# Optimization experiments

Measured on AMD Instinct MI355X. Metric: run time of the kernel, lower is better.

## Reference

```python
import jax, jax.numpy as jnp
import numpy as np

N = 100000      # nodes
E = 3200000     # edges
D_IN = 16
D_OUT = 32
DIM = 3         # pseudo-coordinate dimensionality
K = 2           # kernel_size per dim
NUM_K = K ** DIM  # 8 spline kernel weight matrices
BN_EPS = 1e-5


def _spline_basis(pseudo):
    """Degree-1 open B-spline basis, kernel_size=2 per dim.

    v = pseudo * (K - degree) = pseudo, so for pseudo in [0,1) floor(v)=0 and
    frac = pseudo; per-dim basis over the 2 knots is (1-frac, frac). The full
    basis over all 2^DIM kernel weights is the outer product across dims,
    flattened with flat index = i0 + 2*i1 + 4*i2.
    Returns [E, 2^DIM].
    """
    frac = pseudo  # [E, DIM]
    e = pseudo.shape[0]
    basis = jnp.ones((e, 1), pseudo.dtype)
    for d in range(DIM):
        b_d = jnp.stack([1.0 - frac[:, d], frac[:, d]], axis=1)  # [E, 2]
        # new flat index = i_d * prev_size + prev_index
        basis = (basis[:, None, :] * b_d[:, :, None]).reshape(e, -1)
    return basis  # [E, NUM_K]


def setup_inputs() -> dict:
    key = jax.random.key(0)
    ks = jax.random.split(key, 6)
    x = jax.random.normal(ks[0], (N, D_IN), dtype=jnp.float32)
    edge_index = jax.random.randint(ks[1], (2, E), 0, N, dtype=jnp.int32)
    edge_attr = jax.random.uniform(ks[2], (E, DIM), dtype=jnp.float32)
    # learned params
    W = jax.random.normal(ks[3], (NUM_K, D_IN, D_OUT), dtype=jnp.float32) * 0.1
    W_root = jax.random.normal(ks[4], (D_IN, D_OUT), dtype=jnp.float32) * 0.1
    bias = jnp.zeros((D_OUT,), jnp.float32)
    gamma = jnp.ones((D_OUT,), jnp.float32)
    beta = jnp.zeros((D_OUT,), jnp.float32)
    return dict(x=x, edge_index=edge_index, edge_attr=edge_attr,
                W=W, W_root=W_root, bias=bias, gamma=gamma, beta=beta)


def reference(x, edge_index, edge_attr, W, W_root, bias, gamma, beta):
    src, dst = edge_index[0], edge_index[1]
    basis = _spline_basis(edge_attr)          # [E, 8]
    x_j = x[src]                              # [E, d_in] per-edge gather
    # basis-weighted linear combination over the 8 kernel weights
    msg = jnp.zeros((x_j.shape[0], D_OUT), x.dtype)
    for k in range(NUM_K):                    # fixed small loop over kernels
        msg = msg + basis[:, k:k + 1] * (x_j @ W[k])
    # scatter-mean to target nodes (SplineConv default aggr='mean')
    agg = jax.ops.segment_sum(msg, dst, num_segments=N)
    cnt = jax.ops.segment_sum(jnp.ones((msg.shape[0],), x.dtype), dst, num_segments=N)
    agg = agg / jnp.maximum(cnt, 1.0)[:, None]
    out = agg + x @ W_root + bias             # root weight + bias
    out = jax.nn.elu(out)                     # activation
    # BatchNorm over the node dimension (training mode: batch statistics)
    mean = out.mean(axis=0)
    var = out.var(axis=0)
    out = (out - mean) * jax.lax.rsqrt(var + BN_EPS) * gamma + beta
    return out
```

## Files before the change

kernel.cpp:

```cpp
#include <hip/hip_runtime.h>
#include <math.h>

#define TPB 256
#define FTPB 512
#define D_IN 16
#define D_OUT 32
#define NUM_K 8
#define WPAD 516
#define SBN_LOG 9
#define SBN 512
#define CT 4096
#define EPT 16

__global__ void k_init(int* __restrict__ sbase, int* __restrict__ scursor,
                       int* __restrict__ sbcnt, int cap, int strided) {
    int t = threadIdx.x;
    if (t < 257) sbase[t] = strided ? t * cap : 0;
    if (t < 256) { scursor[t] = 0; sbcnt[t] = 0; }
}


__global__ void k_sbhist(const int* __restrict__ dst, int* __restrict__ sbcnt, int E) {
    __shared__ int h[256];
    for (int i = threadIdx.x; i < 256; i += TPB) h[i] = 0;
    __syncthreads();
    int stride = gridDim.x * TPB;
    for (int e = blockIdx.x * TPB + threadIdx.x; e < E; e += stride)
        atomicAdd(&h[dst[e] >> SBN_LOG], 1);
    __syncthreads();
    for (int i = threadIdx.x; i < 256; i += TPB)
        if (h[i]) atomicAdd(&sbcnt[i], h[i]);
}

__global__ void k_sbscan(const int* __restrict__ sbcnt, int* __restrict__ sbase, int nsb) {
    __shared__ int sd[256];
    int t = threadIdx.x;
    int own = (t < nsb) ? sbcnt[t] : 0;
    sd[t] = own;
    __syncthreads();
    for (int s = 1; s < 256; s <<= 1) {
        int add = (t >= s) ? sd[t - s] : 0;
        __syncthreads();
        sd[t] += add;
        __syncthreads();
    }
    sbase[t] = sd[t] - own;
}

__global__ __launch_bounds__(TPB) void k_coarse(
        const int* __restrict__ src, const int* __restrict__ dst,
        const float* __restrict__ attr, const int* __restrict__ sbase,
        int* __restrict__ scursor, uint2* __restrict__ tmp, int E, int nsb) {
    __shared__ int hist[256];
    __shared__ int base[256];
    __shared__ int goff[256];
    __shared__ __align__(16) uint2 stage[CT];
    __shared__ unsigned char ssb[CT];

    int tile0 = blockIdx.x * CT;
    for (int i = threadIdx.x; i < 256; i += TPB) hist[i] = 0;
    __syncthreads();

    unsigned rx[EPT], ry[EPT];
    int rk[EPT], sbv[EPT];
#pragma unroll
    for (int i = 0; i < EPT; i++) {
        int e = tile0 + i * TPB + threadIdx.x;
        sbv[i] = -1;
        if (e < E) {
            int s = src[e], d = dst[e];
            float f0 = attr[3 * e + 0], f1 = attr[3 * e + 1], f2 = attr[3 * e + 2];
            int q0 = min((int)(f0 * 1024.f), 1023);
            int q1 = min((int)(f1 * 1024.f), 1023);
            int q2 = min((int)(f2 * 1024.f), 1023);
            int sb = d >> SBN_LOG;
            rx[i] = (unsigned)s | ((unsigned)(d & (SBN - 1)) << 17);
            ry[i] = (unsigned)q0 | ((unsigned)q1 << 10) | ((unsigned)q2 << 20);
            rk[i] = atomicAdd(&hist[sb], 1);
            sbv[i] = sb;
        }
    }
    __syncthreads();

    int t = threadIdx.x;
    int cntv = hist[t];
    base[t] = cntv;
    __syncthreads();
    for (int s = 1; s < 256; s <<= 1) {
        int add = (t >= s) ? base[t - s] : 0;
        __syncthreads();
        base[t] += add;
        __syncthreads();
    }
    int excl = base[t] - cntv;
    if (t < nsb && cntv > 0) goff[t] = sbase[t] + atomicAdd(&scursor[t], cntv);
    __syncthreads();
    base[t] = excl;
    __syncthreads();

#pragma unroll
    for (int i = 0; i < EPT; i++) {
        if (sbv[i] >= 0) {
            int slot = base[sbv[i]] + rk[i];
            stage[slot] = make_uint2(rx[i], ry[i]);
            ssb[slot] = (unsigned char)sbv[i];
        }
    }
    __syncthreads();

    int tileCount = min(E - tile0, CT);
    for (int j = threadIdx.x; j < tileCount; j += TPB) {
        int sb = ssb[j];
        tmp[goff[sb] + (j - base[sb])] = stage[j];
    }
}

__global__ __launch_bounds__(FTPB) void k_fine2(
        const uint2* __restrict__ tmp, const int* __restrict__ sbase,
        const int* __restrict__ scursor, int* __restrict__ rs, int* __restrict__ re,
        uint2* __restrict__ rec, int N) {
    __shared__ int hist[SBN];
    __shared__ int wsum[8], woff[8];
    int b = blockIdx.x;
    int lo = sbase[b];
    int hi = lo + scursor[b];
    int t = threadIdx.x;
    hist[t] = 0;
    __syncthreads();
    for (int p = lo + t; p < hi; p += FTPB)
        atomicAdd(&hist[(tmp[p].x >> 17) & (SBN - 1)], 1);
    __syncthreads();
    int own = hist[t];

    int lane = t & 63, w = t >> 6;
    int inc = own;
#pragma unroll
    for (int s = 1; s < 64; s <<= 1) {
        int u = __shfl_up(inc, s);
        if (lane >= s) inc += u;
    }
    if (lane == 63) wsum[w] = inc;
    __syncthreads();
    if (t < 8) {
        int x = wsum[t], ex = x;
#pragma unroll
        for (int s = 1; s < 8; s <<= 1) {
            int u = __shfl_up(ex, s);
            if (t >= s) ex += u;
        }
        woff[t] = ex - x;
    }
    __syncthreads();
    int incl = inc + woff[w];
    int excl = incl - own;

    int n = (b << SBN_LOG) + t;
    if (n < N) { rs[n] = lo + excl; re[n] = lo + incl; }
    hist[t] = lo + excl;
    __syncthreads();
    for (int p = lo + t; p < hi; p += FTPB) {
        uint2 r = tmp[p];
        int dl = (int)((r.x >> 17) & (SBN - 1));
        int slot = atomicAdd(&hist[dl], 1);
        rec[slot] = make_uint2(r.x & 0x1FFFFu, r.y);
    }
}


__global__ void k_zero(int* __restrict__ cnt, int N) {
    int i = blockIdx.x * TPB + threadIdx.x;
    if (i < N) cnt[i] = 0;
}

__global__ void k_hist(const int* __restrict__ dst, int* __restrict__ cnt, int E) {
    int e = blockIdx.x * TPB + threadIdx.x;
    if (e < E) atomicAdd(&cnt[dst[e]], 1);
}

__global__ void k_scan_a(const int* __restrict__ cnt, int* __restrict__ bsum, int N) {
    __shared__ int sd[TPB];
    int i = blockIdx.x * TPB + threadIdx.x;
    sd[threadIdx.x] = (i < N) ? cnt[i] : 0;
    __syncthreads();
    for (int s = TPB / 2; s > 0; s >>= 1) {
        if (threadIdx.x < s) sd[threadIdx.x] += sd[threadIdx.x + s];
        __syncthreads();
    }
    if (threadIdx.x == 0) bsum[blockIdx.x] = sd[0];
}

__global__ void k_scan_b(const int* __restrict__ bsum, int* __restrict__ boff, int nb) {
    __shared__ int sd[512];
    int t = threadIdx.x;
    int own = (t < nb) ? bsum[t] : 0;
    sd[t] = own;
    __syncthreads();
    for (int s = 1; s < 512; s <<= 1) {
        int a = sd[t];
        int b = (t >= s) ? sd[t - s] : 0;
        __syncthreads();
        sd[t] = a + b;
        __syncthreads();
    }
    if (t < nb) boff[t] = sd[t] - own;
}

__global__ void k_scan_c(const int* __restrict__ cnt, const int* __restrict__ boff,
                         int* __restrict__ rs, int* __restrict__ re, int N) {
    __shared__ int sd[TPB];
    int t = threadIdx.x;
    int i = blockIdx.x * TPB + t;
    int v = (i < N) ? cnt[i] : 0;
    sd[t] = v;
    __syncthreads();
    for (int s = 1; s < TPB; s <<= 1) {
        int a = sd[t];
        int b = (t >= s) ? sd[t - s] : 0;
        __syncthreads();
        sd[t] = a + b;
        __syncthreads();
    }
    int excl = sd[t] - v + boff[blockIdx.x];
    if (i < N) { rs[i] = excl; re[i] = excl; }
}

__global__ void k_scatter(const int* __restrict__ src, const int* __restrict__ dst,
                          const float* __restrict__ attr, int* __restrict__ re,
                          uint2* __restrict__ rec, int E) {
    int e = blockIdx.x * TPB + threadIdx.x;
    if (e < E) {
        float f0 = attr[3 * e + 0], f1 = attr[3 * e + 1], f2 = attr[3 * e + 2];
        int q0 = min((int)(f0 * 1024.f), 1023);
        int q1 = min((int)(f1 * 1024.f), 1023);
        int q2 = min((int)(f2 * 1024.f), 1023);
        unsigned pk = (unsigned)q0 | ((unsigned)q1 << 10) | ((unsigned)q2 << 20);
        int pos = atomicAdd(&re[dst[e]], 1);
        rec[pos] = make_uint2((unsigned)src[e], pk);
    }
}


__global__ __launch_bounds__(TPB, 4) void k_agg(
    const float* __restrict__ x, const float* __restrict__ W,
    const float* __restrict__ Wr, const float* __restrict__ bias,
    const int* __restrict__ rs, const int* __restrict__ re,
    const uint2* __restrict__ rec,
    float* __restrict__ out, float* __restrict__ partials, int N) {

    __shared__ __align__(16) float sW[NUM_K * WPAD];
    __shared__ __align__(16) float sWr[D_IN * D_OUT];
    __shared__ float sB[D_OUT];
    __shared__ float4 sStats[4][16];

    for (int idx = threadIdx.x; idx < NUM_K * D_IN * D_OUT; idx += TPB) {
        int k = idx >> 9, rem = idx & 511, i = rem >> 5, c = rem & 31;
        sW[k * WPAD + i * 32 + c] = W[idx];
    }
    for (int idx = threadIdx.x; idx < D_IN * D_OUT; idx += TPB) sWr[idx] = Wr[idx];
    if (threadIdx.x < D_OUT) sB[threadIdx.x] = bias[threadIdx.x];
    __syncthreads();

    int t   = blockIdx.x * TPB + threadIdx.x;
    int n   = t >> 4;
    int sub = t & 15;
    int grp = sub >> 3;
    int h   = sub & 7;
    bool valid = n < N;

    const float INV = 1.0f / 1024.0f, HLF = 1.0f / 2048.0f;
    float sc0 = (h & 1) ? INV : -INV, cc0 = (h & 1) ? HLF : 1.f - HLF;
    float sc1 = (h & 2) ? INV : -INV, cc1 = (h & 2) ? HLF : 1.f - HLF;
    float sc2 = (h & 4) ? INV : -INV, cc2 = (h & 4) ? HLF : 1.f - HLF;

    float4 g0 = {0,0,0,0}, g1 = {0,0,0,0}, g2 = {0,0,0,0}, g3 = {0,0,0,0};
    int deg = 0;
    if (valid) {
        int p0 = rs[n], p1 = re[n];
        deg = p1 - p0;
        int p = p0 + grp;
        if (p < p1) {
            int last = p1 - 1;
            uint2 r  = rec[p];
            uint2 rn = rec[min(p + 2, last)];
            const float4* xr = (const float4*)x + (size_t)r.x * 4;
            float4 xq0 = xr[0], xq1 = xr[1], xq2 = xr[2], xq3 = xr[3];
            for (; p < p1; p += 2) {
                uint2 rnn = rec[min(p + 4, last)];
                const float4* xnr = (const float4*)x + (size_t)rn.x * 4;
                float4 xn0 = xnr[0], xn1 = xnr[1], xn2 = xnr[2], xn3 = xnr[3];
                float q0v = (float)(r.y & 1023u);
                float q1v = (float)((r.y >> 10) & 1023u);
                float q2v = (float)((r.y >> 20) & 1023u);
                float bs = fmaf(q0v, sc0, cc0) * fmaf(q1v, sc1, cc1) * fmaf(q2v, sc2, cc2);
                g0.x = fmaf(bs, xq0.x, g0.x); g0.y = fmaf(bs, xq0.y, g0.y);
                g0.z = fmaf(bs, xq0.z, g0.z); g0.w = fmaf(bs, xq0.w, g0.w);
                g1.x = fmaf(bs, xq1.x, g1.x); g1.y = fmaf(bs, xq1.y, g1.y);
                g1.z = fmaf(bs, xq1.z, g1.z); g1.w = fmaf(bs, xq1.w, g1.w);
                g2.x = fmaf(bs, xq2.x, g2.x); g2.y = fmaf(bs, xq2.y, g2.y);
                g2.z = fmaf(bs, xq2.z, g2.z); g2.w = fmaf(bs, xq2.w, g2.w);
                g3.x = fmaf(bs, xq3.x, g3.x); g3.y = fmaf(bs, xq3.y, g3.y);
                g3.z = fmaf(bs, xq3.z, g3.z); g3.w = fmaf(bs, xq3.w, g3.w);
                r = rn; rn = rnn;
                xq0 = xn0; xq1 = xn1; xq2 = xn2; xq3 = xn3;
            }
        }
    }

    g0.x += __shfl_xor(g0.x, 8); g0.y += __shfl_xor(g0.y, 8);
    g0.z += __shfl_xor(g0.z, 8); g0.w += __shfl_xor(g0.w, 8);
    g1.x += __shfl_xor(g1.x, 8); g1.y += __shfl_xor(g1.y, 8);
    g1.z += __shfl_xor(g1.z, 8); g1.w += __shfl_xor(g1.w, 8);
    g2.x += __shfl_xor(g2.x, 8); g2.y += __shfl_xor(g2.y, 8);
    g2.z += __shfl_xor(g2.z, 8); g2.w += __shfl_xor(g2.w, 8);
    g3.x += __shfl_xor(g3.x, 8); g3.y += __shfl_xor(g3.y, 8);
    g3.z += __shfl_xor(g3.z, 8); g3.w += __shfl_xor(g3.w, 8);

    float4 o0 = {0,0,0,0}, o1 = {0,0,0,0}, o2 = {0,0,0,0}, o3 = {0,0,0,0};
    const float* wbase = sW + h * WPAD + grp * 16;
#define CONTRACT1(gv, i) { \
        const float4* wr_ = (const float4*)(wbase + (i) * 32); \
        float4 w0 = wr_[0], w1 = wr_[1], w2 = wr_[2], w3 = wr_[3]; \
        o0.x = fmaf(gv, w0.x, o0.x); o0.y = fmaf(gv, w0.y, o0.y); \
        o0.z = fmaf(gv, w0.z, o0.z); o0.w = fmaf(gv, w0.w, o0.w); \
        o1.x = fmaf(gv, w1.x, o1.x); o1.y = fmaf(gv, w1.y, o1.y); \
        o1.z = fmaf(gv, w1.z, o1.z); o1.w = fmaf(gv, w1.w, o1.w); \
        o2.x = fmaf(gv, w2.x, o2.x); o2.y = fmaf(gv, w2.y, o2.y); \
        o2.z = fmaf(gv, w2.z, o2.z); o2.w = fmaf(gv, w2.w, o2.w); \
        o3.x = fmaf(gv, w3.x, o3.x); o3.y = fmaf(gv, w3.y, o3.y); \
        o3.z = fmaf(gv, w3.z, o3.z); o3.w = fmaf(gv, w3.w, o3.w); }
    CONTRACT1(g0.x,  0) CONTRACT1(g0.y,  1) CONTRACT1(g0.z,  2) CONTRACT1(g0.w,  3)
    CONTRACT1(g1.x,  4) CONTRACT1(g1.y,  5) CONTRACT1(g1.z,  6) CONTRACT1(g1.w,  7)
    CONTRACT1(g2.x,  8) CONTRACT1(g2.y,  9) CONTRACT1(g2.z, 10) CONTRACT1(g2.w, 11)
    CONTRACT1(g3.x, 12) CONTRACT1(g3.y, 13) CONTRACT1(g3.z, 14) CONTRACT1(g3.w, 15)
#undef CONTRACT1

    float inv = 1.f / (float)(deg > 0 ? deg : 1);
    o0.x *= inv; o0.y *= inv; o0.z *= inv; o0.w *= inv;
    o1.x *= inv; o1.y *= inv; o1.z *= inv; o1.w *= inv;
    o2.x *= inv; o2.y *= inv; o2.z *= inv; o2.w *= inv;
    o3.x *= inv; o3.y *= inv; o3.z *= inv; o3.w *= inv;

    bool hi4 = (h & 4) != 0;
    float4 k0, k1, s0, s1;
    k0 = hi4 ? o2 : o0; k1 = hi4 ? o3 : o1;
    s0 = hi4 ? o0 : o2; s1 = hi4 ? o1 : o3;
    k0.x += __shfl_xor(s0.x, 4); k0.y += __shfl_xor(s0.y, 4);
    k0.z += __shfl_xor(s0.z, 4); k0.w += __shfl_xor(s0.w, 4);
    k1.x += __shfl_xor(s1.x, 4); k1.y += __shfl_xor(s1.y, 4);
    k1.z += __shfl_xor(s1.z, 4); k1.w += __shfl_xor(s1.w, 4);

    bool hi2 = (h & 2) != 0;
    float4 m0 = hi2 ? k1 : k0;
    float4 sm = hi2 ? k0 : k1;
    m0.x += __shfl_xor(sm.x, 2); m0.y += __shfl_xor(sm.y, 2);
    m0.z += __shfl_xor(sm.z, 2); m0.w += __shfl_xor(sm.w, 2);

    bool hi1 = (h & 1) != 0;
    float e0 = hi1 ? m0.z : m0.x;
    float e1 = hi1 ? m0.w : m0.y;
    float sa = hi1 ? m0.x : m0.z;
    float sb_ = hi1 ? m0.y : m0.w;
    e0 += __shfl_xor(sa, 1);
    e1 += __shfl_xor(sb_, 1);

    int c0 = 2 * sub;
    if (valid) {
        const float4* xr = (const float4*)x + (size_t)n * 4;
        float4 r0 = xr[0], r1 = xr[1], r2 = xr[2], r3 = xr[3];
#define ROOT1(xv, i) { \
            float2 w = *(const float2*)(sWr + (i) * 32 + c0); \
            e0 = fmaf(xv, w.x, e0); e1 = fmaf(xv, w.y, e1); }
        ROOT1(r0.x,  0) ROOT1(r0.y,  1) ROOT1(r0.z,  2) ROOT1(r0.w,  3)
        ROOT1(r1.x,  4) ROOT1(r1.y,  5) ROOT1(r1.z,  6) ROOT1(r1.w,  7)
        ROOT1(r2.x,  8) ROOT1(r2.y,  9) ROOT1(r2.z, 10) ROOT1(r2.w, 11)
        ROOT1(r3.x, 12) ROOT1(r3.y, 13) ROOT1(r3.z, 14) ROOT1(r3.w, 15)
#undef ROOT1
    }

    float2 bb = *(const float2*)(sB + c0);
    e0 += bb.x; e1 += bb.y;
    e0 = e0 > 0.f ? e0 : (__expf(e0) - 1.f);
    e1 = e1 > 0.f ? e1 : (__expf(e1) - 1.f);

    if (valid) *(float2*)(out + (size_t)n * D_OUT + c0) = make_float2(e0, e1);

    float ss0 = valid ? e0 : 0.f, ss1 = valid ? e1 : 0.f;
    float q0 = ss0 * ss0, q1 = ss1 * ss1;
    ss0 += __shfl_xor(ss0, 16); ss1 += __shfl_xor(ss1, 16);
    q0  += __shfl_xor(q0, 16);  q1  += __shfl_xor(q1, 16);
    ss0 += __shfl_xor(ss0, 32); ss1 += __shfl_xor(ss1, 32);
    q0  += __shfl_xor(q0, 32);  q1  += __shfl_xor(q1, 32);
    if ((threadIdx.x & 63) < 16)
        sStats[threadIdx.x >> 6][sub] = make_float4(ss0, ss1, q0, q1);
    __syncthreads();
    if (threadIdx.x < 64) {
        const float* sf = (const float*)sStats;
        float v = sf[threadIdx.x] + sf[64 + threadIdx.x] +
                  sf[128 + threadIdx.x] + sf[192 + threadIdx.x];
        int ssub = threadIdx.x >> 2, comp = threadIdx.x & 3;
        int col = 2 * ssub + (comp & 1) + 32 * (comp >> 1);
        partials[(size_t)blockIdx.x * 64 + col] = v;
    }
}


__global__ void k_red1(const float* __restrict__ partials, float* __restrict__ partials2,
                       int nrows) {
    __shared__ float sd[4][64];
    int col = threadIdx.x & 63, j = threadIdx.x >> 6;
    float v = 0.f;
    for (int k = 0; k < 16; k++) {
        int r = blockIdx.x * 64 + j * 16 + k;
        if (r < nrows) v += partials[(size_t)r * 64 + col];
    }
    sd[j][col] = v;
    __syncthreads();
    if (threadIdx.x < 64)
        partials2[(size_t)blockIdx.x * 64 + threadIdx.x] =
            sd[0][threadIdx.x] + sd[1][threadIdx.x] + sd[2][threadIdx.x] + sd[3][threadIdx.x];
}

__global__ void k_bnfin(const float* __restrict__ partials2, const float* __restrict__ gamma,
                        const float* __restrict__ beta, float* __restrict__ stats,
                        int nrows2, int N) {
    __shared__ float sd[2][64];
    int col = threadIdx.x & 63, j = threadIdx.x >> 6;
    float v = 0.f;
    for (int r = j; r < nrows2; r += 2) v += partials2[(size_t)r * 64 + col];
    sd[j][col] = v;
    __syncthreads();
    if (threadIdx.x < 32) {
        int c = threadIdx.x;
        float S = sd[0][c] + sd[1][c];
        float Q = sd[0][32 + c] + sd[1][32 + c];
        float mean = S / (float)N;
        float var  = Q / (float)N - mean * mean;
        float sc   = gamma[c] * rsqrtf(var + 1e-5f);
        stats[c]      = sc;
        stats[32 + c] = beta[c] - mean * sc;
    }
}

__global__ void k_bnapply(float* __restrict__ out, const float* __restrict__ stats, int total4) {
    int i = blockIdx.x * TPB + threadIdx.x;
    if (i < total4) {
        float4 v = ((float4*)out)[i];
        int c0 = (i * 4) & (D_OUT - 1);
        v.x = v.x * stats[c0 + 0] + stats[32 + c0 + 0];
        v.y = v.y * stats[c0 + 1] + stats[32 + c0 + 1];
        v.z = v.z * stats[c0 + 2] + stats[32 + c0 + 2];
        v.w = v.w * stats[c0 + 3] + stats[32 + c0 + 3];
        ((float4*)out)[i] = v;
    }
}


extern "C" void kernel_launch(void* const* d_in, const int* in_sizes, int n_in,
                              void* d_out, int out_size, void* d_ws, size_t ws_size,
                              hipStream_t stream) {
    const float* x     = (const float*)d_in[0];
    const int* eidx    = (const int*)d_in[1];
    const float* attr  = (const float*)d_in[2];
    const float* W     = (const float*)d_in[3];
    const float* Wr    = (const float*)d_in[4];
    const float* bias  = (const float*)d_in[5];
    const float* gamma = (const float*)d_in[6];
    const float* beta  = (const float*)d_in[7];
    float* out = (float*)d_out;

    const int N = in_sizes[0] / D_IN;
    const int E = in_sizes[1] / 2;
    const int* src = eidx;
    const int* dst = eidx + E;

    const int nb  = (N + TPB - 1) / TPB;
    const int gE  = (E + TPB - 1) / TPB;
    const int nsb = (N + SBN - 1) / SBN;
    const int nbAgg = (16 * N + TPB - 1) / TPB;
    const int nbRed = (nbAgg + 63) / 64;
    const int gC  = (E + CT - 1) / CT;

    int capBase = (E + nsb - 1) / nsb;
    int slack = capBase / 16 > 1024 ? capBase / 16 : 1024;
    int cap = capBase + slack;

    int* rs          = (int*)d_ws;
    int* re          = rs + N;
    float* partials  = (float*)(re + N);
    float* partials2 = partials + (size_t)nbAgg * 64;
    float* stats     = partials2 + (size_t)nbRed * 64;
    int* sbase       = (int*)(stats + 64);
    int* scursor     = sbase + 257;
    int* sbcnt       = scursor + 256;
    uintptr_t tail   = ((uintptr_t)(sbcnt + 256) + 15) & ~(uintptr_t)15;
    size_t headBytes = tail - (uintptr_t)d_ws;

    size_t recStr      = (size_t)nsb * cap;
    size_t needStrided = headBytes + 2 * recStr * 8;
    size_t needDense   = headBytes + 2 * (size_t)E * 8;
    size_t needSingle  = headBytes + (size_t)E * 8 + ((size_t)N + 2 * (size_t)nb) * 4;

    if (ws_size >= needStrided && nsb <= 256) {
        uint2* rec = (uint2*)tail;
        uint2* tmp = rec + recStr;
        k_init<<<1, 512, 0, stream>>>(sbase, scursor, sbcnt, cap, 1);
        k_coarse<<<gC, TPB, 0, stream>>>(src, dst, attr, sbase, scursor, tmp, E, nsb);
        k_fine2<<<nsb, FTPB, 0, stream>>>(tmp, sbase, scursor, rs, re, rec, N);
        k_agg<<<nbAgg, TPB, 0, stream>>>(x, W, Wr, bias, rs, re, rec, out, partials, N);
    } else if (ws_size >= needDense && nsb <= 256) {
        uint2* rec = (uint2*)tail;
        uint2* tmp = rec + E;
        k_init<<<1, 512, 0, stream>>>(sbase, scursor, sbcnt, cap, 0);
        int gH = min(1024, gE);
        k_sbhist<<<gH, TPB, 0, stream>>>(dst, sbcnt, E);
        k_sbscan<<<1, 256, 0, stream>>>(sbcnt, sbase, nsb);
        k_coarse<<<gC, TPB, 0, stream>>>(src, dst, attr, sbase, scursor, tmp, E, nsb);
        k_fine2<<<nsb, FTPB, 0, stream>>>(tmp, sbase, scursor, rs, re, rec, N);
        k_agg<<<nbAgg, TPB, 0, stream>>>(x, W, Wr, bias, rs, re, rec, out, partials, N);
    } else if (ws_size >= needSingle && nb <= 512) {
        uint2* rec = (uint2*)tail;
        int* cnt   = (int*)(rec + E);
        int* bsum  = cnt + N;
        int* boff  = bsum + nb;
        k_zero<<<nb, TPB, 0, stream>>>(cnt, N);
        k_hist<<<gE, TPB, 0, stream>>>(dst, cnt, E);
        k_scan_a<<<nb, TPB, 0, stream>>>(cnt, bsum, N);
        k_scan_b<<<1, 512, 0, stream>>>(bsum, boff, nb);
        k_scan_c<<<nb, TPB, 0, stream>>>(cnt, boff, rs, re, N);
        k_scatter<<<gE, TPB, 0, stream>>>(src, dst, attr, re, rec, E);
        k_agg<<<nbAgg, TPB, 0, stream>>>(x, W, Wr, bias, rs, re, rec, out, partials, N);
    }

    k_red1<<<nbRed, TPB, 0, stream>>>(partials, partials2, nbAgg);
    k_bnfin<<<1, 128, 0, stream>>>(partials2, gamma, beta, stats, nbRed, N);
    int total4 = N * D_OUT / 4;
    k_bnapply<<<(total4 + TPB - 1) / TPB, TPB, 0, stream>>>(out, stats, total4);
}
```

Before: 193.8 us.

## Use 32 threads per node in aggregation kernel, one output column each

The aggregation kernel now assigns 32 lanes per destination node instead of 16. Four edge groups stride the neighbor list, and each lane computes one output column, so the weight contraction, shuffle tree, root term and stats each carry half as much work per lane. The intent is more memory-level parallelism on the edge gather and lower register pressure per thread. The cost is twice the thread count, an extra shuffle stage to reduce the groups, and twice as many partial-stat rows for the reduction kernels.

After: 203.8 us. 1.05x slower.

```diff
diff --git a/kernel.cpp b/kernel.cpp
--- a/kernel.cpp
+++ b/kernel.cpp
@@ -250,7 +250,7 @@
     __shared__ __align__(16) float sW[NUM_K * WPAD];
     __shared__ __align__(16) float sWr[D_IN * D_OUT];
     __shared__ float sB[D_OUT];
-    __shared__ float4 sStats[4][16];
+    __shared__ float2 sStats[4][32];
 
     for (int idx = threadIdx.x; idx < NUM_K * D_IN * D_OUT; idx += TPB) {
         int k = idx >> 9, rem = idx & 511, i = rem >> 5, c = rem & 31;
@@ -261,8 +261,8 @@
     __syncthreads();
 
     int t   = blockIdx.x * TPB + threadIdx.x;
-    int n   = t >> 4;
-    int sub = t & 15;
+    int n   = t >> 5;
+    int sub = t & 31;
     int grp = sub >> 3;
     int h   = sub & 7;
     bool valid = n < N;
@@ -281,11 +281,11 @@
         if (p < p1) {
             int last = p1 - 1;
             uint2 r  = rec[p];
-            uint2 rn = rec[min(p + 2, last)];
+            uint2 rn = rec[min(p + 4, last)];
             const float4* xr = (const float4*)x + (size_t)r.x * 4;
             float4 xq0 = xr[0], xq1 = xr[1], xq2 = xr[2], xq3 = xr[3];
-            for (; p < p1; p += 2) {
-                uint2 rnn = rec[min(p + 4, last)];
+            for (; p < p1; p += 4) {
+                uint2 rnn = rec[min(p + 8, last)];
                 const float4* xnr = (const float4*)x + (size_t)rn.x * 4;
                 float4 xn0 = xnr[0], xn1 = xnr[1], xn2 = xnr[2], xn3 = xnr[3];
                 float q0v = (float)(r.y & 1023u);
@@ -314,20 +314,24 @@
     g2.z += __shfl_xor(g2.z, 8); g2.w += __shfl_xor(g2.w, 8);
     g3.x += __shfl_xor(g3.x, 8); g3.y += __shfl_xor(g3.y, 8);
     g3.z += __shfl_xor(g3.z, 8); g3.w += __shfl_xor(g3.w, 8);
-
-    float4 o0 = {0,0,0,0}, o1 = {0,0,0,0}, o2 = {0,0,0,0}, o3 = {0,0,0,0};
-    const float* wbase = sW + h * WPAD + grp * 16;
+    g0.x += __shfl_xor(g0.x, 16); g0.y += __shfl_xor(g0.y, 16);
+    g0.z += __shfl_xor(g0.z, 16); g0.w += __shfl_xor(g0.w, 16);
+    g1.x += __shfl_xor(g1.x, 16); g1.y += __shfl_xor(g1.y, 16);
+    g1.z += __shfl_xor(g1.z, 16); g1.w += __shfl_xor(g1.w, 16);
+    g2.x += __shfl_xor(g2.x, 16); g2.y += __shfl_xor(g2.y, 16);
+    g2.z += __shfl_xor(g2.z, 16); g2.w += __shfl_xor(g2.w, 16);
+    g3.x += __shfl_xor(g3.x, 16); g3.y += __shfl_xor(g3.y, 16);
+    g3.z += __shfl_xor(g3.z, 16); g3.w += __shfl_xor(g3.w, 16);
+
+    float4 o0 = {0,0,0,0}, o1 = {0,0,0,0};
+    const float* wbase = sW + h * WPAD + grp * 8;
 #define CONTRACT1(gv, i) { \
         const float4* wr_ = (const float4*)(wbase + (i) * 32); \
-        float4 w0 = wr_[0], w1 = wr_[1], w2 = wr_[2], w3 = wr_[3]; \
+        float4 w0 = wr_[0], w1 = wr_[1]; \
         o0.x = fmaf(gv, w0.x, o0.x); o0.y = fmaf(gv, w0.y, o0.y); \
         o0.z = fmaf(gv, w0.z, o0.z); o0.w = fmaf(gv, w0.w, o0.w); \
         o1.x = fmaf(gv, w1.x, o1.x); o1.y = fmaf(gv, w1.y, o1.y); \
-        o1.z = fmaf(gv, w1.z, o1.z); o1.w = fmaf(gv, w1.w, o1.w); \
-        o2.x = fmaf(gv, w2.x, o2.x); o2.y = fmaf(gv, w2.y, o2.y); \
-        o2.z = fmaf(gv, w2.z, o2.z); o2.w = fmaf(gv, w2.w, o2.w); \
-        o3.x = fmaf(gv, w3.x, o3.x); o3.y = fmaf(gv, w3.y, o3.y); \
-        o3.z = fmaf(gv, w3.z, o3.z); o3.w = fmaf(gv, w3.w, o3.w); }
+        o1.z = fmaf(gv, w1.z, o1.z); o1.w = fmaf(gv, w1.w, o1.w); }
     CONTRACT1(g0.x,  0) CONTRACT1(g0.y,  1) CONTRACT1(g0.z,  2) CONTRACT1(g0.w,  3)
     CONTRACT1(g1.x,  4) CONTRACT1(g1.y,  5) CONTRACT1(g1.z,  6) CONTRACT1(g1.w,  7)
     CONTRACT1(g2.x,  8) CONTRACT1(g2.y,  9) CONTRACT1(g2.z, 10) CONTRACT1(g2.w, 11)
@@ -337,39 +341,30 @@
     float inv = 1.f / (float)(deg > 0 ? deg : 1);
     o0.x *= inv; o0.y *= inv; o0.z *= inv; o0.w *= inv;
     o1.x *= inv; o1.y *= inv; o1.z *= inv; o1.w *= inv;
-    o2.x *= inv; o2.y *= inv; o2.z *= inv; o2.w *= inv;
-    o3.x *= inv; o3.y *= inv; o3.z *= inv; o3.w *= inv;
 
     bool hi4 = (h & 4) != 0;
-    float4 k0, k1, s0, s1;
-    k0 = hi4 ? o2 : o0; k1 = hi4 ? o3 : o1;
-    s0 = hi4 ? o0 : o2; s1 = hi4 ? o1 : o3;
+    float4 k0 = hi4 ? o1 : o0;
+    float4 s0 = hi4 ? o0 : o1;
     k0.x += __shfl_xor(s0.x, 4); k0.y += __shfl_xor(s0.y, 4);
     k0.z += __shfl_xor(s0.z, 4); k0.w += __shfl_xor(s0.w, 4);
-    k1.x += __shfl_xor(s1.x, 4); k1.y += __shfl_xor(s1.y, 4);
-    k1.z += __shfl_xor(s1.z, 4); k1.w += __shfl_xor(s1.w, 4);
 
     bool hi2 = (h & 2) != 0;
-    float4 m0 = hi2 ? k1 : k0;
-    float4 sm = hi2 ? k0 : k1;
-    m0.x += __shfl_xor(sm.x, 2); m0.y += __shfl_xor(sm.y, 2);
-    m0.z += __shfl_xor(sm.z, 2); m0.w += __shfl_xor(sm.w, 2);
+    float mx = hi2 ? k0.z : k0.x;
+    float my = hi2 ? k0.w : k0.y;
+    float sx = hi2 ? k0.x : k0.z;
+    float sy = hi2 ? k0.y : k0.w;
+    mx += __shfl_xor(sx, 2);
+    my += __shfl_xor(sy, 2);
 
     bool hi1 = (h & 1) != 0;
-    float e0 = hi1 ? m0.z : m0.x;
-    float e1 = hi1 ? m0.w : m0.y;
-    float sa = hi1 ? m0.x : m0.z;
-    float sb_ = hi1 ? m0.y : m0.w;
-    e0 += __shfl_xor(sa, 1);
-    e1 += __shfl_xor(sb_, 1);
-
-    int c0 = 2 * sub;
+    float e  = hi1 ? my : mx;
+    float se = hi1 ? mx : my;
+    e += __shfl_xor(se, 1);
+
     if (valid) {
         const float4* xr = (const float4*)x + (size_t)n * 4;
         float4 r0 = xr[0], r1 = xr[1], r2 = xr[2], r3 = xr[3];
-#define ROOT1(xv, i) { \
-            float2 w = *(const float2*)(sWr + (i) * 32 + c0); \
-            e0 = fmaf(xv, w.x, e0); e1 = fmaf(xv, w.y, e1); }
+#define ROOT1(xv, i) e = fmaf(xv, sWr[(i) * 32 + sub], e);
         ROOT1(r0.x,  0) ROOT1(r0.y,  1) ROOT1(r0.z,  2) ROOT1(r0.w,  3)
         ROOT1(r1.x,  4) ROOT1(r1.y,  5) ROOT1(r1.z,  6) ROOT1(r1.w,  7)
         ROOT1(r2.x,  8) ROOT1(r2.y,  9) ROOT1(r2.z, 10) ROOT1(r2.w, 11)
@@ -377,29 +372,26 @@
 #undef ROOT1
     }
 
-    float2 bb = *(const float2*)(sB + c0);
-    e0 += bb.x; e1 += bb.y;
-    e0 = e0 > 0.f ? e0 : (__expf(e0) - 1.f);
-    e1 = e1 > 0.f ? e1 : (__expf(e1) - 1.f);
-
-    if (valid) *(float2*)(out + (size_t)n * D_OUT + c0) = make_float2(e0, e1);
-
-    float ss0 = valid ? e0 : 0.f, ss1 = valid ? e1 : 0.f;
-    float q0 = ss0 * ss0, q1 = ss1 * ss1;
-    ss0 += __shfl_xor(ss0, 16); ss1 += __shfl_xor(ss1, 16);
-    q0  += __shfl_xor(q0, 16);  q1  += __shfl_xor(q1, 16);
-    ss0 += __shfl_xor(ss0, 32); ss1 += __shfl_xor(ss1, 32);
-    q0  += __shfl_xor(q0, 32);  q1  += __shfl_xor(q1, 32);
-    if ((threadIdx.x & 63) < 16)
-        sStats[threadIdx.x >> 6][sub] = make_float4(ss0, ss1, q0, q1);
+    e += sB[sub];
+    e = e > 0.f ? e : (__expf(e) - 1.f);
+
+    if (valid) out[(size_t)n * D_OUT + sub] = e;
+
+    float s = valid ? e : 0.f;
+    float q = s * s;
+    s += __shfl_xor(s, 32);
+    q += __shfl_xor(q, 32);
+    if ((threadIdx.x & 63) < 32)
+        sStats[threadIdx.x >> 6][sub] = make_float2(s, q);
     __syncthreads();
     if (threadIdx.x < 64) {
-        const float* sf = (const float*)sStats;
-        float v = sf[threadIdx.x] + sf[64 + threadIdx.x] +
-                  sf[128 + threadIdx.x] + sf[192 + threadIdx.x];
-        int ssub = threadIdx.x >> 2, comp = threadIdx.x & 3;
-        int col = 2 * ssub + (comp & 1) + 32 * (comp >> 1);
-        partials[(size_t)blockIdx.x * 64 + col] = v;
+        int c = threadIdx.x & 31, which = threadIdx.x >> 5;
+        float v;
+        if (which == 0)
+            v = sStats[0][c].x + sStats[1][c].x + sStats[2][c].x + sStats[3][c].x;
+        else
+            v = sStats[0][c].y + sStats[1][c].y + sStats[2][c].y + sStats[3][c].y;
+        partials[(size_t)blockIdx.x * 64 + which * 32 + c] = v;
     }
 }
 
@@ -476,7 +468,7 @@
     const int nb  = (N + TPB - 1) / TPB;
     const int gE  = (E + TPB - 1) / TPB;
     const int nsb = (N + SBN - 1) / SBN;
-    const int nbAgg = (16 * N + TPB - 1) / TPB;
+    const int nbAgg = (32 * N + TPB - 1) / TPB;
     const int nbRed = (nbAgg + 63) / 64;
     const int gC  = (E + CT - 1) / CT;
 
```
